# Kernel tuning notes

Measured on AMD Instinct MI355X. Metric: run time of the kernel, lower is better.

## Reference

```python
import jax, jax.numpy as jnp
import numpy as np

DIM = 1024
H = 56
NS = 32            # n_state == head_v_dim
KEY_DIM = H * NS   # 1792
D_INNER = H * NS   # 1792
T_LEN = 2048
B = 4


def _xavier(key, fan_out, fan_in):
    bound = (6.0 / (fan_in + fan_out)) ** 0.5
    return jax.random.uniform(key, (fan_out, fan_in), jnp.float32, -bound, bound)


def setup_inputs() -> dict:
    key = jax.random.key(0)
    ks = jax.random.split(key, 8)
    x = jax.random.normal(ks[0], (T_LEN, B, DIM), jnp.float32)
    S = jnp.zeros((B, H, NS, NS), jnp.float32)
    Wq = _xavier(ks[1], KEY_DIM, DIM)
    Wk = _xavier(ks[2], KEY_DIM, DIM)
    Wv = _xavier(ks[3], D_INNER, DIM)
    Wa = _xavier(ks[4], H, DIM)
    Wout = _xavier(ks[5], DIM, D_INNER)
    A_log = jax.random.uniform(ks[6], (H,), jnp.float32, -5.0, -1.0)
    dt_bias = jax.random.uniform(ks[7], (H,), jnp.float32, 0.5, 1.5)
    return {"x": x, "S": S, "Wq": Wq, "Wk": Wk, "Wv": Wv, "Wa": Wa,
            "A_log": A_log, "dt_bias": dt_bias, "Wout": Wout}


def _l2norm(t):
    # matches F.normalize(dim=-1): x / max(||x||, 1e-12)
    n = jnp.sqrt(jnp.sum(t * t, axis=-1, keepdims=True))
    return t / jnp.maximum(n, 1e-12)


def reference(x, S, Wq, Wk, Wv, Wa, A_log, dt_bias, Wout):
    T, Bb, _ = x.shape
    q = jax.nn.silu(x @ Wq.T).reshape(T, Bb, H, NS)
    k = jax.nn.silu(x @ Wk.T).reshape(T, Bb, H, NS)
    v = jax.nn.silu(x @ Wv.T).reshape(T, Bb, H, NS)
    q = _l2norm(q)
    k = _l2norm(k)
    a = x @ Wa.T                                   # [T,B,H]
    dt = jax.nn.softplus(a + dt_bias)
    decay = jnp.exp(-jnp.exp(A_log) * dt)          # [T,B,H]

    def step(S_t, inp):
        k_t, v_t, q_t, d_t = inp                   # [B,H,NS], [B,H,NS], [B,H,NS], [B,H]
        retrieved = jnp.einsum('bhij,bhi->bhj', S_t, k_t)   # S^T k
        delta = v_t - retrieved
        outer = k_t[..., :, None] * delta[..., None, :]     # [B,H,NS,NS] = k ox delta
        S_t = S_t + jnp.tanh(d_t[..., None, None] * S_t + outer)
        Sq = jnp.einsum('bhij,bhi->bhj', S_t, q_t)
        return S_t, Sq

    S_new, out = jax.lax.scan(step, S, (k, v, q, decay))
    out = out.reshape(T, Bb, D_INNER) @ Wout.T     # [T,B,dim]
    return out, S_new
```

## Files before the change

kernel.cpp:

```cpp
#include <hip/hip_runtime.h>


typedef __attribute__((ext_vector_type(8))) __bf16 bf16x8;
typedef __attribute__((ext_vector_type(8))) _Float16 f16x8;
typedef __attribute__((ext_vector_type(4))) float f32x4;
typedef __attribute__((ext_vector_type(2))) unsigned int u32x2;

#define T_LEN 2048
#define BB 4
#define HH 56
#define NS 32
#define DIM 1024
#define KD 1792
#define MROWS 8192
#define CH 16
#define NCHUNK (T_LEN / CH)

#define VMCNT(N) asm volatile("s_waitcnt vmcnt(" #N ")" ::: "memory")
#define LGKM(N)  asm volatile("s_waitcnt lgkmcnt(" #N ")" ::: "memory")
#define SB       __builtin_amdgcn_sched_barrier(0)

__device__ __forceinline__ float bf2f(unsigned short u) {
    return __uint_as_float(((unsigned int)u) << 16);
}
__device__ __forceinline__ unsigned short f2bf(float f) {
    unsigned int u = __float_as_uint(f);
    u += 0x7fffu + ((u >> 16) & 1u);
    return (unsigned short)(u >> 16);
}
__device__ __forceinline__ unsigned short f2h(float f) {
    union { _Float16 h; unsigned short u; } cv;
    cv.h = (_Float16)f;
    return cv.u;
}
__device__ __forceinline__ float h2f(unsigned short u) {
    union { unsigned short u; _Float16 h; } cv;
    cv.u = u;
    return (float)cv.h;
}

__device__ __forceinline__ float tanh_fast(float x) {
    float e = __builtin_amdgcn_exp2f(x * 2.885390081777927f);
    float r = __builtin_amdgcn_rcpf(e + 1.0f);
    return fmaf(-2.0f, r, 1.0f);
}

__device__ __forceinline__ float dpp_sum8(float x) {
    int t;
    t = __builtin_amdgcn_update_dpp(0, __float_as_int(x), 0xB1, 0xf, 0xf, true);
    x += __int_as_float(t);
    t = __builtin_amdgcn_update_dpp(0, __float_as_int(x), 0x4E, 0xf, 0xf, true);
    x += __int_as_float(t);
    t = __builtin_amdgcn_update_dpp(0, __float_as_int(x), 0x141, 0xf, 0xf, true);
    x += __int_as_float(t);
    return x;
}

__device__ __forceinline__ void gload_lds16(const void* g, void* l) {
    __builtin_amdgcn_global_load_lds(
        (const __attribute__((address_space(1))) unsigned int*)g,
        (__attribute__((address_space(3))) unsigned int*)l, 16, 0, 0);
}
__device__ __forceinline__ void gload_lds4(const void* g, void* l) {
    __builtin_amdgcn_global_load_lds(
        (const __attribute__((address_space(1))) unsigned int*)g,
        (__attribute__((address_space(3))) unsigned int*)l, 4, 0, 0);
}

__device__ __forceinline__ unsigned lds_off(const void* p) {
    return (unsigned)(unsigned long long)
        (const __attribute__((address_space(3))) char*)p;
}

template <int OFF>
__device__ __forceinline__ f32x4 dsr128(unsigned a) {
    f32x4 r;
    asm volatile("ds_read_b128 %0, %1 offset:%2" : "=v"(r) : "v"(a), "n"(OFF));
    return r;
}
template <int OFF>
__device__ __forceinline__ u32x2 dsr64(unsigned a) {
    u32x2 r;
    asm volatile("ds_read_b64 %0, %1 offset:%2" : "=v"(r) : "v"(a), "n"(OFF));
    return r;
}
template <int OFF>
__device__ __forceinline__ float dsr32(unsigned a) {
    float r;
    asm volatile("ds_read_b32 %0, %1 offset:%2" : "=v"(r) : "v"(a), "n"(OFF));
    return r;
}

__global__ void cast_split3_kernel(const float* __restrict__ in,
                                   unsigned short* __restrict__ hi,
                                   unsigned short* __restrict__ lo,
                                   unsigned short* __restrict__ h16, int n8) {
    int i = blockIdx.x * blockDim.x + threadIdx.x;
    if (i >= n8) return;
    const float4* p = (const float4*)in + (size_t)i * 2;
    float4 a = p[0], b = p[1];
    float xs[8] = {a.x, a.y, a.z, a.w, b.x, b.y, b.z, b.w};
    unsigned int ho[4], lv[4], hv[4];
#pragma unroll
    for (int c = 0; c < 4; ++c) {
        unsigned short h0 = f2bf(xs[2 * c]);
        unsigned short h1 = f2bf(xs[2 * c + 1]);
        unsigned short l0 = f2bf(xs[2 * c] - bf2f(h0));
        unsigned short l1 = f2bf(xs[2 * c + 1] - bf2f(h1));
        ho[c] = (unsigned int)h0 | ((unsigned int)h1 << 16);
        lv[c] = (unsigned int)l0 | ((unsigned int)l1 << 16);
        hv[c] = (unsigned int)f2h(xs[2 * c]) | ((unsigned int)f2h(xs[2 * c + 1]) << 16);
    }
    ((uint4*)hi)[i]  = (uint4){ho[0], ho[1], ho[2], ho[3]};
    ((uint4*)lo)[i]  = (uint4){lv[0], lv[1], lv[2], lv[3]};
    ((uint4*)h16)[i] = (uint4){hv[0], hv[1], hv[2], hv[3]};
}

__global__ void cast_split_kernel(const float* __restrict__ in,
                                  unsigned short* __restrict__ hi,
                                  unsigned short* __restrict__ lo, int n8) {
    int i = blockIdx.x * blockDim.x + threadIdx.x;
    if (i >= n8) return;
    const float4* p = (const float4*)in + (size_t)i * 2;
    float4 a = p[0], b = p[1];
    float xs[8] = {a.x, a.y, a.z, a.w, b.x, b.y, b.z, b.w};
    unsigned int ho[4], lv[4];
#pragma unroll
    for (int c = 0; c < 4; ++c) {
        unsigned short h0 = f2bf(xs[2 * c]);
        unsigned short h1 = f2bf(xs[2 * c + 1]);
        unsigned short l0 = f2bf(xs[2 * c] - bf2f(h0));
        unsigned short l1 = f2bf(xs[2 * c + 1] - bf2f(h1));
        ho[c] = (unsigned int)h0 | ((unsigned int)h1 << 16);
        lv[c] = (unsigned int)l0 | ((unsigned int)l1 << 16);
    }
    ((uint4*)hi)[i] = (uint4){ho[0], ho[1], ho[2], ho[3]};
    ((uint4*)lo)[i] = (uint4){lv[0], lv[1], lv[2], lv[3]};
}

__global__ void cast_half_kernel(const float* __restrict__ in,
                                 unsigned short* __restrict__ out, int n8) {
    int i = blockIdx.x * blockDim.x + threadIdx.x;
    if (i >= n8) return;
    const float4* p = (const float4*)in + (size_t)i * 2;
    float4 a = p[0], b = p[1];
    uint4 o;
    o.x = (unsigned int)f2h(a.x) | ((unsigned int)f2h(a.y) << 16);
    o.y = (unsigned int)f2h(a.z) | ((unsigned int)f2h(a.w) << 16);
    o.z = (unsigned int)f2h(b.x) | ((unsigned int)f2h(b.y) << 16);
    o.w = (unsigned int)f2h(b.z) | ((unsigned int)f2h(b.w) << 16);
    ((uint4*)out)[i] = o;
}

__device__ __forceinline__ void gemm_split(
    const unsigned short* __restrict__ Ah, const unsigned short* __restrict__ Al,
    const unsigned short* __restrict__ Bh, const unsigned short* __restrict__ Bl,
    int m0, int n0, int K, int bmax,
    unsigned short* AsH, unsigned short* AsL,
    unsigned short* BsH, unsigned short* BsL,
    f32x4 (&acc)[4][4]) {
    const int tid  = threadIdx.x;
    const int lane = tid & 63;
    const int wave = tid >> 6;
    const int wm = wave >> 1, wn = wave & 1;
    const int lr = lane & 15, lkb = lane >> 4;

#pragma unroll
    for (int fr = 0; fr < 4; ++fr)
#pragma unroll
        for (int fc = 0; fc < 4; ++fc) acc[fr][fc] = (f32x4){0.f, 0.f, 0.f, 0.f};

    auto stage = [&](int kt) {
#pragma unroll
        for (int c = 0; c < 2; ++c) {
            int i = c * 256 + tid;
            int r = i >> 2, kk = (i & 3) << 3;
            size_t ao = (size_t)(m0 + r) * K + kt + kk;
            int br = n0 + r; if (br > bmax) br = bmax;
            size_t bo = (size_t)br * K + kt + kk;
            gload_lds16(Ah + ao, AsH + i * 8);
            gload_lds16(Al + ao, AsL + i * 8);
            gload_lds16(Bh + bo, BsH + i * 8);
            gload_lds16(Bl + bo, BsL + i * 8);
        }
    };

    stage(0);
    const int nk = K >> 5;
    for (int t = 0; t < nk; ++t) {
        __syncthreads();
        bf16x8 ah[4], al[4], bh[4], bl[4];
#pragma unroll
        for (int f = 0; f < 4; ++f) {
            int ai = (wm * 64 + f * 16 + lr) * 32 + lkb * 8;
            int bi = (wn * 64 + f * 16 + lr) * 32 + lkb * 8;
            ah[f] = *(const bf16x8*)(AsH + ai);
            al[f] = *(const bf16x8*)(AsL + ai);
            bh[f] = *(const bf16x8*)(BsH + bi);
            bl[f] = *(const bf16x8*)(BsL + bi);
        }
#pragma unroll
        for (int fr = 0; fr < 4; ++fr)
#pragma unroll
            for (int fc = 0; fc < 4; ++fc) {
                acc[fr][fc] = __builtin_amdgcn_mfma_f32_16x16x32_bf16(
                    ah[fr], bh[fc], acc[fr][fc], 0, 0, 0);
                acc[fr][fc] = __builtin_amdgcn_mfma_f32_16x16x32_bf16(
                    ah[fr], bl[fc], acc[fr][fc], 0, 0, 0);
                acc[fr][fc] = __builtin_amdgcn_mfma_f32_16x16x32_bf16(
                    al[fr], bh[fc], acc[fr][fc], 0, 0, 0);
            }
        __syncthreads();
        if (t + 1 < nk) stage((t + 1) << 5);
    }
}

__global__ __launch_bounds__(256) void proj_split_kernel(
    const unsigned short* __restrict__ xh, const unsigned short* __restrict__ xl,
    const unsigned short* __restrict__ Wh, const unsigned short* __restrict__ Wl,
    const unsigned short* __restrict__ Wah, const unsigned short* __restrict__ Wal,
    const float* __restrict__ A_log, const float* __restrict__ dt_bias,
    float* __restrict__ dstF, float* __restrict__ decayb) {
    __shared__ __align__(16) unsigned short AsH[128 * 32];
    __shared__ __align__(16) unsigned short AsL[128 * 32];
    __shared__ __align__(16) unsigned short BsH[128 * 32];
    __shared__ __align__(16) unsigned short BsL[128 * 32];

    const int tile = blockIdx.x;
    const bool isdecay = (tile == 14);
    int m0 = blockIdx.y * 128;
    int n0 = isdecay ? 0 : tile * 128;
    int bmax = isdecay ? (HH - 1) : (KD - 1);
    const unsigned short* Bh = isdecay ? Wah : Wh;
    const unsigned short* Bl = isdecay ? Wal : Wl;

    f32x4 acc[4][4];
    gemm_split(xh, xl, Bh, Bl, m0, n0, DIM, bmax, AsH, AsL, BsH, BsL, acc);

    const int lane = threadIdx.x & 63, wave = threadIdx.x >> 6;
    const int wm = wave >> 1, wn = wave & 1, lr = lane & 15, lkb = lane >> 4;

#pragma unroll
    for (int fr = 0; fr < 4; ++fr)
#pragma unroll
        for (int fc = 0; fc < 4; ++fc)
#pragma unroll
            for (int v = 0; v < 4; ++v) {
                int m = m0 + wm * 64 + fr * 16 + lkb * 4 + v;
                int n = n0 + wn * 64 + fc * 16 + lr;
                int t = m >> 2, b = m & 3;
                float y = acc[fr][fc][v];
                if (!isdecay) {
                    int h = n >> 5, i = n & 31;
                    float s = y / (1.f + __expf(-y));
                    dstF[(((size_t)(b * HH + h)) * T_LEN + t) * NS + i] = s;
                } else if (n < HH) {
                    float z = y + dt_bias[n];
                    float sp = (z > 20.f) ? z : log1pf(__expf(z));
                    decayb[((size_t)(b * HH + n)) * T_LEN + t] =
                        __expf(-__expf(A_log[n]) * sp);
                }
            }
}

__global__ __launch_bounds__(256) void q_gemm_f16_kernel(
    const unsigned short* __restrict__ xf, const unsigned short* __restrict__ Wqf,
    unsigned short* __restrict__ dstH) {
    __shared__ __align__(16) unsigned short As[128 * 32];
    __shared__ __align__(16) unsigned short Bs[128 * 32];
    int m0 = blockIdx.y * 128, n0 = blockIdx.x * 128;

    const int tid  = threadIdx.x;
    const int lane = tid & 63;
    const int wave = tid >> 6;
    const int wm = wave >> 1, wn = wave & 1;
    const int lr = lane & 15, lkb = lane >> 4;

    f32x4 acc[4][4];
#pragma unroll
    for (int fr = 0; fr < 4; ++fr)
#pragma unroll
        for (int fc = 0; fc < 4; ++fc) acc[fr][fc] = (f32x4){0.f, 0.f, 0.f, 0.f};

    auto stage = [&](int kt) {
#pragma unroll
        for (int c = 0; c < 2; ++c) {
            int i = c * 256 + tid;
            int r = i >> 2, kk = (i & 3) << 3;
            gload_lds16(xf + (size_t)(m0 + r) * DIM + kt + kk, As + i * 8);
            gload_lds16(Wqf + (size_t)(n0 + r) * DIM + kt + kk, Bs + i * 8);
        }
    };

    stage(0);
    const int nk = DIM >> 5;
    for (int t = 0; t < nk; ++t) {
        __syncthreads();
        f16x8 af[4], bf[4];
#pragma unroll
        for (int f = 0; f < 4; ++f) {
            af[f] = *(const f16x8*)(As + (wm * 64 + f * 16 + lr) * 32 + lkb * 8);
            bf[f] = *(const f16x8*)(Bs + (wn * 64 + f * 16 + lr) * 32 + lkb * 8);
        }
#pragma unroll
        for (int fr = 0; fr < 4; ++fr)
#pragma unroll
            for (int fc = 0; fc < 4; ++fc)
                acc[fr][fc] = __builtin_amdgcn_mfma_f32_16x16x32_f16(
                    af[fr], bf[fc], acc[fr][fc], 0, 0, 0);
        __syncthreads();
        if (t + 1 < nk) stage((t + 1) << 5);
    }

#pragma unroll
    for (int fr = 0; fr < 4; ++fr)
#pragma unroll
        for (int fc = 0; fc < 4; ++fc)
#pragma unroll
            for (int v = 0; v < 4; ++v) {
                int m = m0 + wm * 64 + fr * 16 + lkb * 4 + v;
                int n = n0 + wn * 64 + fc * 16 + lr;
                int t = m >> 2, b = m & 3, h = n >> 5, i = n & 31;
                float y = acc[fr][fc][v];
                float s = y / (1.f + __expf(-y));
                dstH[(((size_t)(b * HH + h)) * T_LEN + t) * NS + i] = f2h(s);
            }
}

__global__ __launch_bounds__(256) void out_gemm_kernel(
    const unsigned short* __restrict__ Sq, const unsigned short* __restrict__ Wo,
    float* __restrict__ out) {
    __shared__ __align__(16) unsigned short As[128 * 32];
    __shared__ __align__(16) unsigned short Bs[128 * 32];
    int m0 = blockIdx.y * 128, n0 = blockIdx.x * 128;

    const int tid  = threadIdx.x;
    const int lane = tid & 63;
    const int wave = tid >> 6;
    const int wm = wave >> 1, wn = wave & 1;
    const int lr = lane & 15, lkb = lane >> 4;

    f32x4 acc[4][4];
#pragma unroll
    for (int fr = 0; fr < 4; ++fr)
#pragma unroll
        for (int fc = 0; fc < 4; ++fc) acc[fr][fc] = (f32x4){0.f, 0.f, 0.f, 0.f};

    auto stage = [&](int kt) {
#pragma unroll
        for (int c = 0; c < 2; ++c) {
            int i = c * 256 + tid;
            int r = i >> 2, kk = (i & 3) << 3;
            gload_lds16(Sq + (size_t)(m0 + r) * KD + kt + kk, As + i * 8);
            gload_lds16(Wo + (size_t)(n0 + r) * KD + kt + kk, Bs + i * 8);
        }
    };

    stage(0);
    const int nk = KD >> 5;
    for (int t = 0; t < nk; ++t) {
        __syncthreads();
        f16x8 af[4], bf[4];
#pragma unroll
        for (int f = 0; f < 4; ++f) {
            af[f] = *(const f16x8*)(As + (wm * 64 + f * 16 + lr) * 32 + lkb * 8);
            bf[f] = *(const f16x8*)(Bs + (wn * 64 + f * 16 + lr) * 32 + lkb * 8);
        }
#pragma unroll
        for (int fr = 0; fr < 4; ++fr)
#pragma unroll
            for (int fc = 0; fc < 4; ++fc)
                acc[fr][fc] = __builtin_amdgcn_mfma_f32_16x16x32_f16(
                    af[fr], bf[fc], acc[fr][fc], 0, 0, 0);
        __syncthreads();
        if (t + 1 < nk) stage((t + 1) << 5);
    }

#pragma unroll
    for (int fr = 0; fr < 4; ++fr)
#pragma unroll
        for (int fc = 0; fc < 4; ++fc)
#pragma unroll
            for (int v = 0; v < 4; ++v) {
                int m = m0 + wm * 64 + fr * 16 + lkb * 4 + v;
                int n = n0 + wn * 64 + fc * 16 + lr;
                out[(size_t)m * DIM + n] = acc[fr][fc][v];
            }
}

__global__ void l2norm_kernel(float* __restrict__ kf,
                              unsigned short* __restrict__ qh) {
    int g = blockIdx.x * blockDim.x + threadIdx.x;
    const int NG = MROWS * HH;
    if (g >= 2 * NG) return;
    if (g < NG) {
        float* p = kf + (size_t)g * NS;
        float4 u[8];
#pragma unroll
        for (int c = 0; c < 8; ++c) u[c] = ((const float4*)p)[c];
        float ss = 0.f;
#pragma unroll
        for (int c = 0; c < 8; ++c) {
            ss = fmaf(u[c].x, u[c].x, ss); ss = fmaf(u[c].y, u[c].y, ss);
            ss = fmaf(u[c].z, u[c].z, ss); ss = fmaf(u[c].w, u[c].w, ss);
        }
        float sc = 1.f / fmaxf(sqrtf(ss), 1e-12f);
#pragma unroll
        for (int c = 0; c < 8; ++c) {
            u[c].x *= sc; u[c].y *= sc; u[c].z *= sc; u[c].w *= sc;
            ((float4*)p)[c] = u[c];
        }
    } else {
        unsigned short* p = qh + (size_t)(g - NG) * NS;
        uint4 u[4];
#pragma unroll
        for (int c = 0; c < 4; ++c) u[c] = ((const uint4*)p)[c];
        float ss = 0.f;
        auto acc2 = [&](unsigned int w) {
            float a = h2f((unsigned short)(w & 0xffff));
            float b = h2f((unsigned short)(w >> 16));
            ss = fmaf(a, a, ss); ss = fmaf(b, b, ss);
        };
#pragma unroll
        for (int c = 0; c < 4; ++c) { acc2(u[c].x); acc2(u[c].y); acc2(u[c].z); acc2(u[c].w); }
        float sc = 1.f / fmaxf(sqrtf(ss), 1e-12f);
        auto scl = [&](unsigned int w) -> unsigned int {
            unsigned int lo = f2h(h2f((unsigned short)(w & 0xffff)) * sc);
            unsigned int hi = f2h(h2f((unsigned short)(w >> 16)) * sc);
            return lo | (hi << 16);
        };
#pragma unroll
        for (int c = 0; c < 4; ++c) {
            u[c].x = scl(u[c].x); u[c].y = scl(u[c].y);
            u[c].z = scl(u[c].z); u[c].w = scl(u[c].w);
            ((uint4*)p)[c] = u[c];
        }
    }
}

__global__ __launch_bounds__(256, 1) void scan_kernel(
    const float* __restrict__ kf, const unsigned short* __restrict__ qh,
    const float* __restrict__ vf, const float* __restrict__ decayb,
    const float* __restrict__ S0, unsigned short* __restrict__ Sq,
    float* __restrict__ Sout) {
    __shared__ __align__(16) float          kbuf[4][CH][NS];
    __shared__ __align__(16) float          vbuf[4][CH][NS];
    __shared__ __align__(16) unsigned short qbuf[4][CH][NS];
    __shared__ __align__(16) float          dbuf[4][64];

    const int bh = blockIdx.x;
    const int b = bh / HH, h = bh - b * HH;
    const int tid = threadIdx.x;
    const int lane = tid & 63, wave = tid >> 6;
    const int j = tid >> 3, sub = tid & 7, i0 = sub << 2;

    const float* Sp = S0 + (size_t)bh * NS * NS;
    float s0 = Sp[(i0 + 0) * NS + j];
    float s1 = Sp[(i0 + 1) * NS + j];
    float s2 = Sp[(i0 + 2) * NS + j];
    float s3 = Sp[(i0 + 3) * NS + j];

    const size_t base  = (size_t)bh * T_LEN * NS;
    const size_t dbase = (size_t)bh * T_LEN;
    const size_t cbcol = (size_t)h * NS;

    const unsigned kb0 = lds_off(&kbuf[0][0][i0]);
    const unsigned qb0 = lds_off(&qbuf[0][0][i0]);
    const unsigned vb0 = lds_off(&vbuf[0][0][j]);
    const unsigned db0 = lds_off(&dbuf[0][0]);

    auto stage = [&](int c) {
        int s = c & 3;
        if (wave == 0) {
            const float* src = kf + base + (size_t)c * CH * NS;
            gload_lds16(src + lane * 4,       &kbuf[s][0][0] + lane * 4);
            gload_lds16(src + 256 + lane * 4, &kbuf[s][8][0] + lane * 4);
        } else if (wave == 1) {
            const float* src = vf + base + (size_t)c * CH * NS;
            gload_lds16(src + lane * 4,       &vbuf[s][0][0] + lane * 4);
            gload_lds16(src + 256 + lane * 4, &vbuf[s][8][0] + lane * 4);
        } else if (wave == 2) {
            const unsigned short* src = qh + base + (size_t)c * CH * NS;
            gload_lds16(src + lane * 8, &qbuf[s][0][0] + lane * 8);
        } else {
            const float* src = decayb + dbase + (size_t)c * CH;
            gload_lds4(src + lane, &dbuf[s][0] + lane);
        }
    };

    stage(0);
    stage(1);
    VMCNT(0);
    __builtin_amdgcn_s_barrier();

    for (int c = 0; c < NCHUNK; ++c) {
        if (c + 2 < NCHUNK) stage(c + 2);
        if (wave < 2) { VMCNT(18); } else { VMCNT(17); }
        __builtin_amdgcn_s_barrier();
        SB;

        const int s = c & 3;
        const unsigned kb = kb0 + (unsigned)s * (CH * NS * 4);
        const unsigned qb = qb0 + (unsigned)s * (CH * NS * 2);
        const unsigned vb = vb0 + (unsigned)s * (CH * NS * 4);
        const unsigned db = db0 + (unsigned)s * 256;

        f32x4 kA[4], kB[4]; u32x2 qA[4], qB[4]; float vA[4], vB[4];
        f32x4 dA, dB;

#define LDG(KK, QQ, VV, DV, g)                                          \
        KK[0] = dsr128<((g) * 4 + 0) * 128>(kb);                        \
        KK[1] = dsr128<((g) * 4 + 1) * 128>(kb);                        \
        KK[2] = dsr128<((g) * 4 + 2) * 128>(kb);                        \
        KK[3] = dsr128<((g) * 4 + 3) * 128>(kb);                        \
        QQ[0] = dsr64<((g) * 4 + 0) * 64>(qb);                          \
        QQ[1] = dsr64<((g) * 4 + 1) * 64>(qb);                          \
        QQ[2] = dsr64<((g) * 4 + 2) * 64>(qb);                          \
        QQ[3] = dsr64<((g) * 4 + 3) * 64>(qb);                          \
        VV[0] = dsr32<((g) * 4 + 0) * 128>(vb);                         \
        VV[1] = dsr32<((g) * 4 + 1) * 128>(vb);                         \
        VV[2] = dsr32<((g) * 4 + 2) * 128>(vb);                         \
        VV[3] = dsr32<((g) * 4 + 3) * 128>(vb);                         \
        DV    = dsr128<(g) * 16>(db);

#define CMP(KK, QQ, VV, DV, g)                                          \
        {                                                               \
            _Pragma("unroll")                                           \
            for (int p = 0; p < 4; ++p) {                               \
                const int t = c * CH + (g) * 4 + p;                     \
                float k0 = KK[p][0], k1 = KK[p][1];                     \
                float k2 = KK[p][2], k3 = KK[p][3];                     \
                float q0 = h2f((unsigned short)(QQ[p][0] & 0xffff));    \
                float q1 = h2f((unsigned short)(QQ[p][0] >> 16));       \
                float q2 = h2f((unsigned short)(QQ[p][1] & 0xffff));    \
                float q3 = h2f((unsigned short)(QQ[p][1] >> 16));       \
                float vj = VV[p];                                       \
                float d  = DV[p];                                       \
                float r = fmaf(k1, s1, k0 * s0) + fmaf(k3, s3, k2 * s2);\
                r = dpp_sum8(r);                                        \
                float delta = vj - r;                                   \
                float a0 = fmaf(d, s0, k0 * delta);                     \
                float a1 = fmaf(d, s1, k1 * delta);                     \
                float a2 = fmaf(d, s2, k2 * delta);                     \
                float a3 = fmaf(d, s3, k3 * delta);                     \
                s0 += tanh_fast(a0); s1 += tanh_fast(a1);               \
                s2 += tanh_fast(a2); s3 += tanh_fast(a3);               \
                float o = fmaf(q1, s1, q0 * s0) + fmaf(q3, s3, q2 * s2);\
                o = dpp_sum8(o);                                        \
                if (sub == 0) {                                         \
                    size_t ro = ((size_t)t * BB + b) * KD + cbcol;      \
                    Sq[ro + j] = f2h(o);                                \
                }                                                       \
            }                                                           \
        }

        LDG(kA, qA, vA, dA, 0);
        LDG(kB, qB, vB, dB, 1);
        LGKM(13); SB;
        CMP(kA, qA, vA, dA, 0);
        LDG(kA, qA, vA, dA, 2);
        LGKM(13); SB;
        CMP(kB, qB, vB, dB, 1);
        LDG(kB, qB, vB, dB, 3);
        LGKM(13); SB;
        CMP(kA, qA, vA, dA, 2);
        LGKM(0); SB;
        CMP(kB, qB, vB, dB, 3);
#undef LDG
#undef CMP
    }

    float* so = Sout + (size_t)bh * NS * NS;
    so[(i0 + 0) * NS + j] = s0;
    so[(i0 + 1) * NS + j] = s1;
    so[(i0 + 2) * NS + j] = s2;
    so[(i0 + 3) * NS + j] = s3;
}

extern "C" void kernel_launch(void* const* d_in, const int* in_sizes, int n_in,
                              void* d_out, int out_size, void* d_ws, size_t ws_size,
                              hipStream_t stream) {
    const float* x       = (const float*)d_in[0];
    const float* S0      = (const float*)d_in[1];
    const float* Wq      = (const float*)d_in[2];
    const float* Wk      = (const float*)d_in[3];
    const float* Wv      = (const float*)d_in[4];
    const float* Wa      = (const float*)d_in[5];
    const float* A_log   = (const float*)d_in[6];
    const float* dt_bias = (const float*)d_in[7];
    const float* Wout    = (const float*)d_in[8];

    float* out  = (float*)d_out;
    float* Sout = out + (size_t)T_LEN * BB * DIM;

    char* w = (char*)d_ws;
    auto alloc = [&](size_t bytes) {
        char* p = w; w += (bytes + 255) & ~(size_t)255; return p;
    };
    unsigned short* xh  = (unsigned short*)alloc((size_t)MROWS * DIM * 2);
    unsigned short* xl  = (unsigned short*)alloc((size_t)MROWS * DIM * 2);
    unsigned short* Wbh = (unsigned short*)alloc((size_t)KD * DIM * 2);
    unsigned short* Wbl = (unsigned short*)alloc((size_t)KD * DIM * 2);
    unsigned short* Wah = (unsigned short*)alloc((size_t)HH * DIM * 2);
    unsigned short* Wal = (unsigned short*)alloc((size_t)HH * DIM * 2);
    float* kf           = (float*)alloc((size_t)MROWS * KD * 4);
    float* vf           = (float*)alloc((size_t)MROWS * KD * 4);
    unsigned short* Woh = (unsigned short*)alloc((size_t)DIM * KD * 2);
    unsigned short* Sq   = xh;
    unsigned short* xf16 = (unsigned short*)vf;

    unsigned short* qh  = (unsigned short*)d_out;
    float* decayb       = (float*)((char*)d_out + (size_t)MROWS * KD * 2);

    {
        int n8 = (int)((size_t)MROWS * DIM / 8);
        cast_split3_kernel<<<(n8 + 255) / 256, 256, 0, stream>>>(x, xh, xl, xf16, n8);
    }
    {
        int n8 = (int)((size_t)KD * DIM / 8);
        cast_half_kernel<<<(n8 + 255) / 256, 256, 0, stream>>>(Wq, Wbh, n8);
        q_gemm_f16_kernel<<<dim3(14, 64), 256, 0, stream>>>(xf16, Wbh, qh);
    }
    {
        int n8 = (int)((size_t)KD * DIM / 8);
        cast_split_kernel<<<(n8 + 255) / 256, 256, 0, stream>>>(Wk, Wbh, Wbl, n8);
        int n8a = (int)((size_t)HH * DIM / 8);
        cast_split_kernel<<<(n8a + 255) / 256, 256, 0, stream>>>(Wa, Wah, Wal, n8a);
        proj_split_kernel<<<dim3(15, 64), 256, 0, stream>>>(
            xh, xl, Wbh, Wbl, Wah, Wal, A_log, dt_bias, kf, decayb);
    }
    {
        int n8 = (int)((size_t)KD * DIM / 8);
        cast_split_kernel<<<(n8 + 255) / 256, 256, 0, stream>>>(Wv, Wbh, Wbl, n8);
        proj_split_kernel<<<dim3(14, 64), 256, 0, stream>>>(
            xh, xl, Wbh, Wbl, Wah, Wal, A_log, dt_bias, vf, decayb);
    }
    {
        int n8 = (int)((size_t)DIM * KD / 8);
        cast_half_kernel<<<(n8 + 255) / 256, 256, 0, stream>>>(Wout, Woh, n8);
    }
    l2norm_kernel<<<(2 * MROWS * HH + 255) / 256, 256, 0, stream>>>(kf, qh);
    scan_kernel<<<BB * HH, 256, 0, stream>>>(kf, qh, vf, decayb, S0, Sq, Sout);
    out_gemm_kernel<<<dim3(8, 64), 256, 0, stream>>>(Sq, Woh, out);
}
```

Before: 805.2 us.

## Fuse L2 norm into projection epilogues and widen scan to 512 threads

Removes the standalone l2norm kernel by computing the per-head L2 norm inside the q and k GEMM epilogues. A 16-lane DPP reduction spans the two 16-column fragments that make up one 32-wide head. The scan kernel now runs 512 threads per (b,h) block, with each thread holding 2 state elements instead of 4. That shortens the serial per-step dependency chain, and chunk staging is spread over six waves. The cost is an extra DPP stage in every per-step reduction and more waves to synchronise per chunk.

```diff
diff --git a/kernel.cpp b/kernel.cpp
--- a/kernel.cpp
+++ b/kernel.cpp
@@ -4,7 +4,7 @@
 typedef __attribute__((ext_vector_type(8))) __bf16 bf16x8;
 typedef __attribute__((ext_vector_type(8))) _Float16 f16x8;
 typedef __attribute__((ext_vector_type(4))) float f32x4;
-typedef __attribute__((ext_vector_type(2))) unsigned int u32x2;
+typedef __attribute__((ext_vector_type(2))) float f32x2;
 
 #define T_LEN 2048
 #define BB 4
@@ -45,7 +45,7 @@
     return fmaf(-2.0f, r, 1.0f);
 }
 
-__device__ __forceinline__ float dpp_sum8(float x) {
+__device__ __forceinline__ float dpp_sum16(float x) {
     int t;
     t = __builtin_amdgcn_update_dpp(0, __float_as_int(x), 0xB1, 0xf, 0xf, true);
     x += __int_as_float(t);
@@ -53,6 +53,8 @@
     x += __int_as_float(t);
     t = __builtin_amdgcn_update_dpp(0, __float_as_int(x), 0x141, 0xf, 0xf, true);
     x += __int_as_float(t);
+    t = __builtin_amdgcn_update_dpp(0, __float_as_int(x), 0x140, 0xf, 0xf, true);
+    x += __int_as_float(t);
     return x;
 }
 
@@ -79,13 +81,19 @@
     return r;
 }
 template <int OFF>
-__device__ __forceinline__ u32x2 dsr64(unsigned a) {
-    u32x2 r;
+__device__ __forceinline__ f32x2 dsr64f(unsigned a) {
+    f32x2 r;
     asm volatile("ds_read_b64 %0, %1 offset:%2" : "=v"(r) : "v"(a), "n"(OFF));
     return r;
 }
 template <int OFF>
-__device__ __forceinline__ float dsr32(unsigned a) {
+__device__ __forceinline__ unsigned dsr32u(unsigned a) {
+    unsigned r;
+    asm volatile("ds_read_b32 %0, %1 offset:%2" : "=v"(r) : "v"(a), "n"(OFF));
+    return r;
+}
+template <int OFF>
+__device__ __forceinline__ float dsr32f(unsigned a) {
     float r;
     asm volatile("ds_read_b32 %0, %1 offset:%2" : "=v"(r) : "v"(a), "n"(OFF));
     return r;
@@ -220,7 +228,7 @@
     const unsigned short* __restrict__ Wh, const unsigned short* __restrict__ Wl,
     const unsigned short* __restrict__ Wah, const unsigned short* __restrict__ Wal,
     const float* __restrict__ A_log, const float* __restrict__ dt_bias,
-    float* __restrict__ dstF, float* __restrict__ decayb) {
+    float* __restrict__ dstF, float* __restrict__ decayb, int knorm) {
     __shared__ __align__(16) unsigned short AsH[128 * 32];
     __shared__ __align__(16) unsigned short AsL[128 * 32];
     __shared__ __align__(16) unsigned short BsH[128 * 32];
@@ -240,27 +248,63 @@
     const int lane = threadIdx.x & 63, wave = threadIdx.x >> 6;
     const int wm = wave >> 1, wn = wave & 1, lr = lane & 15, lkb = lane >> 4;
 
-#pragma unroll
-    for (int fr = 0; fr < 4; ++fr)
-#pragma unroll
-        for (int fc = 0; fc < 4; ++fc)
-#pragma unroll
-            for (int v = 0; v < 4; ++v) {
-                int m = m0 + wm * 64 + fr * 16 + lkb * 4 + v;
-                int n = n0 + wn * 64 + fc * 16 + lr;
-                int t = m >> 2, b = m & 3;
-                float y = acc[fr][fc][v];
-                if (!isdecay) {
+    if (isdecay) {
+#pragma unroll
+        for (int fr = 0; fr < 4; ++fr)
+#pragma unroll
+            for (int fc = 0; fc < 4; ++fc)
+#pragma unroll
+                for (int v = 0; v < 4; ++v) {
+                    int m = m0 + wm * 64 + fr * 16 + lkb * 4 + v;
+                    int n = n0 + wn * 64 + fc * 16 + lr;
+                    int t = m >> 2, b = m & 3;
+                    if (n < HH) {
+                        float z = acc[fr][fc][v] + dt_bias[n];
+                        float sp = (z > 20.f) ? z : log1pf(__expf(z));
+                        decayb[((size_t)(b * HH + n)) * T_LEN + t] =
+                            __expf(-__expf(A_log[n]) * sp);
+                    }
+                }
+        return;
+    }
+
+    if (knorm) {
+#pragma unroll
+        for (int fr = 0; fr < 4; ++fr)
+#pragma unroll
+            for (int hc = 0; hc < 2; ++hc)
+#pragma unroll
+                for (int v = 0; v < 4; ++v) {
+                    float yA = acc[fr][2 * hc][v];
+                    float yB = acc[fr][2 * hc + 1][v];
+                    float sA = yA / (1.f + __expf(-yA));
+                    float sB = yB / (1.f + __expf(-yB));
+                    float ss = fmaf(sA, sA, sB * sB);
+                    ss = dpp_sum16(ss);
+                    float sc = 1.f / fmaxf(sqrtf(ss), 1e-12f);
+                    int m = m0 + wm * 64 + fr * 16 + lkb * 4 + v;
+                    int t = m >> 2, b = m & 3;
+                    int h = ((n0 + wn * 64) >> 5) + hc;
+                    size_t ro = (((size_t)(b * HH + h)) * T_LEN + t) * NS;
+                    dstF[ro + lr]      = sA * sc;
+                    dstF[ro + lr + 16] = sB * sc;
+                }
+    } else {
+#pragma unroll
+        for (int fr = 0; fr < 4; ++fr)
+#pragma unroll
+            for (int fc = 0; fc < 4; ++fc)
+#pragma unroll
+                for (int v = 0; v < 4; ++v) {
+                    int m = m0 + wm * 64 + fr * 16 + lkb * 4 + v;
+                    int n = n0 + wn * 64 + fc * 16 + lr;
+                    int t = m >> 2, b = m & 3;
                     int h = n >> 5, i = n & 31;
+                    float y = acc[fr][fc][v];
                     float s = y / (1.f + __expf(-y));
                     dstF[(((size_t)(b * HH + h)) * T_LEN + t) * NS + i] = s;
-                } else if (n < HH) {
-                    float z = y + dt_bias[n];
-                    float sp = (z > 20.f) ? z : log1pf(__expf(z));
-                    decayb[((size_t)(b * HH + n)) * T_LEN + t] =
-                        __expf(-__expf(A_log[n]) * sp);
                 }
-            }
+    }
 }
 
 __global__ __launch_bounds__(256) void q_gemm_f16_kernel(
@@ -315,15 +359,22 @@
 #pragma unroll
     for (int fr = 0; fr < 4; ++fr)
 #pragma unroll
-        for (int fc = 0; fc < 4; ++fc)
+        for (int hc = 0; hc < 2; ++hc)
 #pragma unroll
             for (int v = 0; v < 4; ++v) {
+                float yA = acc[fr][2 * hc][v];
+                float yB = acc[fr][2 * hc + 1][v];
+                float sA = yA / (1.f + __expf(-yA));
+                float sB = yB / (1.f + __expf(-yB));
+                float ss = fmaf(sA, sA, sB * sB);
+                ss = dpp_sum16(ss);
+                float sc = 1.f / fmaxf(sqrtf(ss), 1e-12f);
                 int m = m0 + wm * 64 + fr * 16 + lkb * 4 + v;
-                int n = n0 + wn * 64 + fc * 16 + lr;
-                int t = m >> 2, b = m & 3, h = n >> 5, i = n & 31;
-                float y = acc[fr][fc][v];
-                float s = y / (1.f + __expf(-y));
-                dstH[(((size_t)(b * HH + h)) * T_LEN + t) * NS + i] = f2h(s);
+                int t = m >> 2, b = m & 3;
+                int h = ((n0 + wn * 64) >> 5) + hc;
+                size_t ro = (((size_t)(b * HH + h)) * T_LEN + t) * NS;
+                dstH[ro + lr]      = f2h(sA * sc);
+                dstH[ro + lr + 16] = f2h(sB * sc);
             }
 }
 
@@ -388,57 +439,7 @@
             }
 }
 
-__global__ void l2norm_kernel(float* __restrict__ kf,
-                              unsigned short* __restrict__ qh) {
-    int g = blockIdx.x * blockDim.x + threadIdx.x;
-    const int NG = MROWS * HH;
-    if (g >= 2 * NG) return;
-    if (g < NG) {
-        float* p = kf + (size_t)g * NS;
-        float4 u[8];
-#pragma unroll
-        for (int c = 0; c < 8; ++c) u[c] = ((const float4*)p)[c];
-        float ss = 0.f;
-#pragma unroll
-        for (int c = 0; c < 8; ++c) {
-            ss = fmaf(u[c].x, u[c].x, ss); ss = fmaf(u[c].y, u[c].y, ss);
-            ss = fmaf(u[c].z, u[c].z, ss); ss = fmaf(u[c].w, u[c].w, ss);
-        }
-        float sc = 1.f / fmaxf(sqrtf(ss), 1e-12f);
-#pragma unroll
-        for (int c = 0; c < 8; ++c) {
-            u[c].x *= sc; u[c].y *= sc; u[c].z *= sc; u[c].w *= sc;
-            ((float4*)p)[c] = u[c];
-        }
-    } else {
-        unsigned short* p = qh + (size_t)(g - NG) * NS;
-        uint4 u[4];
-#pragma unroll
-        for (int c = 0; c < 4; ++c) u[c] = ((const uint4*)p)[c];
-        float ss = 0.f;
-        auto acc2 = [&](unsigned int w) {
-            float a = h2f((unsigned short)(w & 0xffff));
-            float b = h2f((unsigned short)(w >> 16));
-            ss = fmaf(a, a, ss); ss = fmaf(b, b, ss);
-        };
-#pragma unroll
-        for (int c = 0; c < 4; ++c) { acc2(u[c].x); acc2(u[c].y); acc2(u[c].z); acc2(u[c].w); }
-        float sc = 1.f / fmaxf(sqrtf(ss), 1e-12f);
-        auto scl = [&](unsigned int w) -> unsigned int {
-            unsigned int lo = f2h(h2f((unsigned short)(w & 0xffff)) * sc);
-            unsigned int hi = f2h(h2f((unsigned short)(w >> 16)) * sc);
-            return lo | (hi << 16);
-        };
-#pragma unroll
-        for (int c = 0; c < 4; ++c) {
-            u[c].x = scl(u[c].x); u[c].y = scl(u[c].y);
-            u[c].z = scl(u[c].z); u[c].w = scl(u[c].w);
-            ((uint4*)p)[c] = u[c];
-        }
-    }
-}
-
-__global__ __launch_bounds__(256, 1) void scan_kernel(
+__global__ __launch_bounds__(512, 1) void scan_kernel(
     const float* __restrict__ kf, const unsigned short* __restrict__ qh,
     const float* __restrict__ vf, const float* __restrict__ decayb,
     const float* __restrict__ S0, unsigned short* __restrict__ Sq,
@@ -452,39 +453,43 @@
     const int b = bh / HH, h = bh - b * HH;
     const int tid = threadIdx.x;
     const int lane = tid & 63, wave = tid >> 6;
-    const int j = tid >> 3, sub = tid & 7, i0 = sub << 2;
+    const int col = tid >> 4;
+    const int ii  = tid & 15;
+    const int i0  = ii * 2;
 
     const float* Sp = S0 + (size_t)bh * NS * NS;
-    float s0 = Sp[(i0 + 0) * NS + j];
-    float s1 = Sp[(i0 + 1) * NS + j];
-    float s2 = Sp[(i0 + 2) * NS + j];
-    float s3 = Sp[(i0 + 3) * NS + j];
+    float s0 = Sp[(i0 + 0) * NS + col];
+    float s1 = Sp[(i0 + 1) * NS + col];
 
     const size_t base  = (size_t)bh * T_LEN * NS;
     const size_t dbase = (size_t)bh * T_LEN;
     const size_t cbcol = (size_t)h * NS;
 
-    const unsigned kb0 = lds_off(&kbuf[0][0][i0]);
-    const unsigned qb0 = lds_off(&qbuf[0][0][i0]);
-    const unsigned vb0 = lds_off(&vbuf[0][0][j]);
+    const unsigned kb0 = lds_off(&kbuf[0][0][0]) + (unsigned)ii * 8;
+    const unsigned qb0 = lds_off(&qbuf[0][0][0]) + (unsigned)ii * 4;
+    const unsigned vb0 = lds_off(&vbuf[0][0][0]) + (unsigned)col * 4;
     const unsigned db0 = lds_off(&dbuf[0][0]);
 
     auto stage = [&](int c) {
         int s = c & 3;
         if (wave == 0) {
-            const float* src = kf + base + (size_t)c * CH * NS;
-            gload_lds16(src + lane * 4,       &kbuf[s][0][0] + lane * 4);
-            gload_lds16(src + 256 + lane * 4, &kbuf[s][8][0] + lane * 4);
+            gload_lds16(kf + base + (size_t)c * 512 + lane * 4,
+                        &kbuf[s][0][0] + lane * 4);
         } else if (wave == 1) {
-            const float* src = vf + base + (size_t)c * CH * NS;
-            gload_lds16(src + lane * 4,       &vbuf[s][0][0] + lane * 4);
-            gload_lds16(src + 256 + lane * 4, &vbuf[s][8][0] + lane * 4);
+            gload_lds16(kf + base + (size_t)c * 512 + 256 + lane * 4,
+                        &kbuf[s][8][0] + lane * 4);
         } else if (wave == 2) {
-            const unsigned short* src = qh + base + (size_t)c * CH * NS;
-            gload_lds16(src + lane * 8, &qbuf[s][0][0] + lane * 8);
-        } else {
-            const float* src = decayb + dbase + (size_t)c * CH;
-            gload_lds4(src + lane, &dbuf[s][0] + lane);
+            gload_lds16(vf + base + (size_t)c * 512 + lane * 4,
+                        &vbuf[s][0][0] + lane * 4);
+        } else if (wave == 3) {
+            gload_lds16(vf + base + (size_t)c * 512 + 256 + lane * 4,
+                        &vbuf[s][8][0] + lane * 4);
+        } else if (wave == 4) {
+            gload_lds16(qh + base + (size_t)c * 512 + lane * 8,
+                        &qbuf[s][0][0] + lane * 8);
+        } else if (wave == 5) {
+            gload_lds4(decayb + dbase + (size_t)c * CH + lane,
+                       &dbuf[s][0] + lane);
         }
     };
 
@@ -495,7 +500,7 @@
 
     for (int c = 0; c < NCHUNK; ++c) {
         if (c + 2 < NCHUNK) stage(c + 2);
-        if (wave < 2) { VMCNT(18); } else { VMCNT(17); }
+        if (wave < 6) { VMCNT(18); } else { VMCNT(16); }
         __builtin_amdgcn_s_barrier();
         SB;
 
@@ -505,22 +510,22 @@
         const unsigned vb = vb0 + (unsigned)s * (CH * NS * 4);
         const unsigned db = db0 + (unsigned)s * 256;
 
-        f32x4 kA[4], kB[4]; u32x2 qA[4], qB[4]; float vA[4], vB[4];
+        f32x2 kA[4], kB[4]; unsigned qA[4], qB[4]; float vA[4], vB[4];
         f32x4 dA, dB;
 
 #define LDG(KK, QQ, VV, DV, g)                                          \
-        KK[0] = dsr128<((g) * 4 + 0) * 128>(kb);                        \
-        KK[1] = dsr128<((g) * 4 + 1) * 128>(kb);                        \
-        KK[2] = dsr128<((g) * 4 + 2) * 128>(kb);                        \
-        KK[3] = dsr128<((g) * 4 + 3) * 128>(kb);                        \
-        QQ[0] = dsr64<((g) * 4 + 0) * 64>(qb);                          \
-        QQ[1] = dsr64<((g) * 4 + 1) * 64>(qb);                          \
-        QQ[2] = dsr64<((g) * 4 + 2) * 64>(qb);                          \
-        QQ[3] = dsr64<((g) * 4 + 3) * 64>(qb);                          \
-        VV[0] = dsr32<((g) * 4 + 0) * 128>(vb);                         \
-        VV[1] = dsr32<((g) * 4 + 1) * 128>(vb);                         \
-        VV[2] = dsr32<((g) * 4 + 2) * 128>(vb);                         \
-        VV[3] = dsr32<((g) * 4 + 3) * 128>(vb);                         \
+        KK[0] = dsr64f<((g) * 4 + 0) * 128>(kb);                        \
+        KK[1] = dsr64f<((g) * 4 + 1) * 128>(kb);                        \
+        KK[2] = dsr64f<((g) * 4 + 2) * 128>(kb);                        \
+        KK[3] = dsr64f<((g) * 4 + 3) * 128>(kb);                        \
+        QQ[0] = dsr32u<((g) * 4 + 0) * 64>(qb);                         \
+        QQ[1] = dsr32u<((g) * 4 + 1) * 64>(qb);                         \
+        QQ[2] = dsr32u<((g) * 4 + 2) * 64>(qb);                         \
+        QQ[3] = dsr32u<((g) * 4 + 3) * 64>(qb);                         \
+        VV[0] = dsr32f<((g) * 4 + 0) * 128>(vb);                        \
+        VV[1] = dsr32f<((g) * 4 + 1) * 128>(vb);                        \
+        VV[2] = dsr32f<((g) * 4 + 2) * 128>(vb);                        \
+        VV[3] = dsr32f<((g) * 4 + 3) * 128>(vb);                        \
         DV    = dsr128<(g) * 16>(db);
 
 #define CMP(KK, QQ, VV, DV, g)                                          \
@@ -529,27 +534,21 @@
             for (int p = 0; p < 4; ++p) {                               \
                 const int t = c * CH + (g) * 4 + p;                     \
                 float k0 = KK[p][0], k1 = KK[p][1];                     \
-                float k2 = KK[p][2], k3 = KK[p][3];                     \
-                float q0 = h2f((unsigned short)(QQ[p][0] & 0xffff));    \
-                float q1 = h2f((unsigned short)(QQ[p][0] >> 16));       \
-                float q2 = h2f((unsigned short)(QQ[p][1] & 0xffff));    \
-                float q3 = h2f((unsigned short)(QQ[p][1] >> 16));       \
+                float q0 = h2f((unsigned short)(QQ[p] & 0xffff));       \
+                float q1 = h2f((unsigned short)(QQ[p] >> 16));          \
                 float vj = VV[p];                                       \
                 float d  = DV[p];                                       \
-                float r = fmaf(k1, s1, k0 * s0) + fmaf(k3, s3, k2 * s2);\
-                r = dpp_sum8(r);                                        \
+                float r = fmaf(k1, s1, k0 * s0);                        \
+                r = dpp_sum16(r);                                       \
                 float delta = vj - r;                                   \
                 float a0 = fmaf(d, s0, k0 * delta);                     \
                 float a1 = fmaf(d, s1, k1 * delta);                     \
-                float a2 = fmaf(d, s2, k2 * delta);                     \
-                float a3 = fmaf(d, s3, k3 * delta);                     \
                 s0 += tanh_fast(a0); s1 += tanh_fast(a1);               \
-                s2 += tanh_fast(a2); s3 += tanh_fast(a3);               \
-                float o = fmaf(q1, s1, q0 * s0) + fmaf(q3, s3, q2 * s2);\
-                o = dpp_sum8(o);                                        \
-                if (sub == 0) {                                         \
+                float o = fmaf(q1, s1, q0 * s0);                        \
+                o = dpp_sum16(o);                                       \
+                if (ii == 0) {                                          \
                     size_t ro = ((size_t)t * BB + b) * KD + cbcol;      \
-                    Sq[ro + j] = f2h(o);                                \
+                    Sq[ro + col] = f2h(o);                              \
                 }                                                       \
             }                                                           \
         }
@@ -571,10 +570,8 @@
     }
 
     float* so = Sout + (size_t)bh * NS * NS;
-    so[(i0 + 0) * NS + j] = s0;
-    so[(i0 + 1) * NS + j] = s1;
-    so[(i0 + 2) * NS + j] = s2;
-    so[(i0 + 3) * NS + j] = s3;
+    so[(i0 + 0) * NS + col] = s0;
+    so[(i0 + 1) * NS + col] = s1;
 }
 
 extern "C" void kernel_launch(void* const* d_in, const int* in_sizes, int n_in,
@@ -627,19 +624,18 @@
         int n8a = (int)((size_t)HH * DIM / 8);
         cast_split_kernel<<<(n8a + 255) / 256, 256, 0, stream>>>(Wa, Wah, Wal, n8a);
         proj_split_kernel<<<dim3(15, 64), 256, 0, stream>>>(
-            xh, xl, Wbh, Wbl, Wah, Wal, A_log, dt_bias, kf, decayb);
+            xh, xl, Wbh, Wbl, Wah, Wal, A_log, dt_bias, kf, decayb, 1);
     }
     {
         int n8 = (int)((size_t)KD * DIM / 8);
         cast_split_kernel<<<(n8 + 255) / 256, 256, 0, stream>>>(Wv, Wbh, Wbl, n8);
         proj_split_kernel<<<dim3(14, 64), 256, 0, stream>>>(
-            xh, xl, Wbh, Wbl, Wah, Wal, A_log, dt_bias, vf, decayb);
+            xh, xl, Wbh, Wbl, Wah, Wal, A_log, dt_bias, vf, decayb, 0);
     }
     {
         int n8 = (int)((size_t)DIM * KD / 8);
         cast_half_kernel<<<(n8 + 255) / 256, 256, 0, stream>>>(Wout, Woh, n8);
     }
-    l2norm_kernel<<<(2 * MROWS * HH + 255) / 256, 256, 0, stream>>>(kf, qh);
-    scan_kernel<<<BB * HH, 256, 0, stream>>>(kf, qh, vf, decayb, S0, Sq, Sout);
+    scan_kernel<<<BB * HH, 512, 0, stream>>>(kf, qh, vf, decayb, S0, Sq, Sout);
     out_gemm_kernel<<<dim3(8, 64), 256, 0, stream>>>(Sq, Woh, out);
 }
```

Result: faster. 739.7 us (-8.1%).
